# Performance work log

Hardware: AMD Instinct MI355X
Metric: run time of the kernel (lower is better)

Reference implementation:

```python
import jax, jax.numpy as jnp
import numpy as np

S, B, E = 2048, 8, 1024  # seq_len, batch, embed_dim
GAMMA = 0.5              # Kernel(gamma=0.5)


def setup_inputs() -> dict:
    key = jax.random.key(0)
    ks = jax.random.split(key, 4)
    # Weight scale 1/E keeps pairwise squared distances O(1) so the RBF
    # kernel weights are well-conditioned (exp doesn't underflow to all-zeros).
    w_scale = 1.0 / E
    inputs = jax.random.normal(ks[0], (S, B, E), dtype=jnp.float32)
    Wq = jax.random.normal(ks[1], (E, E), dtype=jnp.float32) * w_scale
    Wk = jax.random.normal(ks[2], (E, E), dtype=jnp.float32) * w_scale
    Wv = jax.random.normal(ks[3], (E, E), dtype=jnp.float32) * w_scale
    bq = jnp.zeros((E,), jnp.float32)
    bk = jnp.zeros((E,), jnp.float32)
    bv = jnp.zeros((E,), jnp.float32)
    return {"inputs": inputs, "Wq": Wq, "bq": bq, "Wk": Wk, "bk": bk,
            "Wv": Wv, "bv": bv}


def reference(inputs, Wq, bq, Wk, bk, Wv, bv):
    # QKV projections (nn.Linear: x @ W.T + b)
    q = inputs @ Wq.T + bq  # (S, B, E)
    k = inputs @ Wk.T + bk  # (S, B, E)
    v = inputs @ Wv.T + bv  # (S, B, E)

    # Pairwise RBF kernel sim[t, j, b] = exp(-gamma * ||q[t,b] - k[j,b]||^2)
    # (vectorized replacement of the original O(S^2) python double loop),
    # via ||q||^2 + ||k||^2 - 2 q.k expansion (GEMM-shaped contraction).
    q2 = jnp.sum(q * q, axis=-1)                 # (S, B)
    k2 = jnp.sum(k * k, axis=-1)                 # (S, B)
    qk = jnp.einsum('tbe,jbe->tjb', q, k)        # (S, S, B)
    d2 = q2[:, None, :] + k2[None, :, :] - 2.0 * qk
    d2 = jnp.maximum(d2, 0.0)

    # sim / sim.sum(dim=1) with sim = exp(-gamma*d2) is exactly
    # softmax(-gamma*d2) over axis 1 (the j axis) -- numerically stable form.
    sim = jax.nn.softmax(-GAMMA * d2, axis=1)    # (S, S, B): (t, j, b)

    # Aggregate values: out[t, b, e] = sum_j sim[t, j, b] * v[j, b, e]
    return jnp.einsum('tjb,jbe->tbe', sim, v)    # (S, B, E)
```

## Files before the change

kernel.cpp:

```cpp
#include <hip/hip_runtime.h>
#include <stdint.h>

#define S_LEN 2048
#define BATCH 8
#define EMB   1024
#define GAMMA 0.5f

typedef unsigned short ushort_t;
typedef __attribute__((ext_vector_type(8))) short  short8;
typedef __attribute__((ext_vector_type(8))) unsigned short ushort8;
typedef __attribute__((ext_vector_type(4))) float  floatx4;

__device__ __forceinline__ ushort_t f2bf(float f) {
  uint32_t x = __float_as_uint(f);
  x += 0x7fffu + ((x >> 16) & 1u);
  return (ushort_t)(x >> 16);
}

__device__ __forceinline__ void gl_lds16(const ushort_t* g, ushort_t* l) {
  __builtin_amdgcn_global_load_lds(
      (const __attribute__((address_space(1))) unsigned int*)g,
      (__attribute__((address_space(3))) unsigned int*)l, 16, 0, 0);
}


#define MFMA_16(AR, B0, B1, J0, J1)                                            \
  _Pragma("unroll")                                                            \
  for (int i = 0; i < 8; ++i) {                                                \
    acc[i][J0] = __builtin_amdgcn_mfma_f32_16x16x32_bf16(AR[i], B0, acc[i][J0], 0, 0, 0); \
    acc[i][J1] = __builtin_amdgcn_mfma_f32_16x16x32_bf16(AR[i], B1, acc[i][J1], 0, 0, 0); \
  }

#define PHASE_END()                                                            \
  asm volatile("s_waitcnt lgkmcnt(0)" ::: "memory");                           \
  __builtin_amdgcn_s_barrier();                                                \
  asm volatile("" ::: "memory");

__device__ __forceinline__ void gemm8_core(
    const ushort_t* __restrict__ A, const ushort_t* __restrict__ B,
    int lda, int ldb, int K, ushort_t* smem, floatx4 (&acc)[8][4])
{
  const int tid = threadIdx.x;
  const int wave = tid >> 6, lane = tid & 63;
  const int wm = wave >> 2, wn = wave & 3;
  const int lr = lane & 15, q = lane >> 4;
  const int NT = K >> 6;
  const int ra = wm * 128 + lr;
  const int rb = wn * 64 + lr;
  const int r4 = lane >> 2;
  const int slot = (lane & 3) ^ ((r4 >> 1) & 3);
  ushort_t* const lw = smem + wave * 1024;

  const int aOff = ra * 32 + (((q ^ (ra >> 1)) & 3) << 3);
  const int bOff = rb * 32 + (((q ^ (rb >> 1)) & 3) << 3);

  const ushort_t* pA0 = A + (size_t)(wave * 32 + r4) * lda + slot * 8;
  const ushort_t* pA1 = pA0 + (size_t)16 * lda;
  const ushort_t* pB0 = B + (size_t)(wave * 32 + r4) * ldb + slot * 8;
  const ushort_t* pB1 = pB0 + (size_t)16 * ldb;

  auto stA = [&](int regionOff, int koff) {
    gl_lds16(pA0 + koff, lw + regionOff);
    gl_lds16(pA1 + koff, lw + regionOff + 512);
  };
  auto stB = [&](int regionOff, int koff) {
    gl_lds16(pB0 + koff, lw + regionOff);
    gl_lds16(pB1 + koff, lw + regionOff + 512);
  };

  stA(0, 0);      stB(16384, 0);
  stA(8192, 32);  stB(24576, 32);
  stA(32768, 64); stB(49152, 64);
  stA(40960, 96);
  asm volatile("s_waitcnt vmcnt(6)" ::: "memory");
  __builtin_amdgcn_s_barrier();
  asm volatile("" ::: "memory");

  short8 ar[8], ar2[8], b0, b1, t0, t1, u0, u1;
  {
    const ushort_t* pa = smem + aOff;
    const ushort_t* pb = smem + 16384 + bOff;
#pragma unroll
    for (int i = 0; i < 8; ++i) ar[i] = *(const short8*)(pa + i * 512);
    b0 = *(const short8*)(pb);
    b1 = *(const short8*)(pb + 512);
  }

  for (int kt = 0; kt < NT; ++kt) {
    const int bo = (kt & 1) * 32768;
    const int bn = bo ^ 32768;
    const ushort_t* const curA0 = smem + bo + aOff;
    const ushort_t* const curA1 = smem + bo + 8192 + aOff;
    const ushort_t* const curB0 = smem + bo + 16384 + bOff;
    const ushort_t* const curB1 = smem + bo + 24576 + bOff;
    const ushort_t* const nxtA0 = smem + bn + aOff;
    const ushort_t* const nxtB0 = smem + bn + 16384 + bOff;
    const bool s1 = (kt + 1) < NT, s2 = (kt + 2) < NT;
    const int k1 = (kt + 1) << 6, k2 = (kt + 2) << 6;

    t0 = *(const short8*)(curB0 + 1024);
    t1 = *(const short8*)(curB0 + 1536);
#pragma unroll
    for (int i = 0; i < 4; ++i) ar2[i] = *(const short8*)(curA1 + i * 512);
    if (s1) stB(bn + 24576, k1 + 32);
    __builtin_amdgcn_s_setprio(1);
    MFMA_16(ar, b0, b1, 0, 1)
    __builtin_amdgcn_s_setprio(0);
    PHASE_END()

#pragma unroll
    for (int i = 4; i < 8; ++i) ar2[i] = *(const short8*)(curA1 + i * 512);
    u0 = *(const short8*)(curB1);
    u1 = *(const short8*)(curB1 + 512);
    if (s2) stA(bo, k2);
    __builtin_amdgcn_s_setprio(1);
    MFMA_16(ar, t0, t1, 2, 3)
    __builtin_amdgcn_s_setprio(0);
    PHASE_END()

    t0 = *(const short8*)(curB1 + 1024);
    t1 = *(const short8*)(curB1 + 1536);
    if (s2) stB(bo + 16384, k2);
    __builtin_amdgcn_s_setprio(1);
    MFMA_16(ar2, u0, u1, 0, 1)
    __builtin_amdgcn_s_setprio(0);
    if (s2)      { asm volatile("s_waitcnt vmcnt(4)" ::: "memory"); }
    else if (s1) { asm volatile("s_waitcnt vmcnt(0)" ::: "memory"); }
    PHASE_END()

    if (s1) {
#pragma unroll
      for (int i = 0; i < 8; ++i) ar[i] = *(const short8*)(nxtA0 + i * 512);
      b0 = *(const short8*)(nxtB0);
      b1 = *(const short8*)(nxtB0 + 512);
    }
    if (s2) stA(bo + 8192, k2 + 32);
    __builtin_amdgcn_s_setprio(1);
    MFMA_16(ar2, t0, t1, 2, 3)
    __builtin_amdgcn_s_setprio(0);
    PHASE_END()
  }
}

__global__ __launch_bounds__(256) void k_quant_x(const float* __restrict__ X,
                                                 ushort_t* __restrict__ Xb) {
  size_t i = ((size_t)blockIdx.x * 256 + threadIdx.x) * 4;
  float4 v = *(const float4*)(X + i);
  *(ushort4*)(Xb + i) = make_ushort4(f2bf(v.x), f2bf(v.y), f2bf(v.z), f2bf(v.w));
}

__global__ __launch_bounds__(256) void k_quant_w(
    const float* __restrict__ Wq, const float* __restrict__ Wk,
    const float* __restrict__ Wv, ushort_t* __restrict__ W) {
  size_t i = ((size_t)blockIdx.x * 256 + threadIdx.x) * 4;
  int row = (int)(i >> 10), col = (int)(i & 1023);
  int sel = row >> 10, sr = row & 1023;
  const float* src = sel == 0 ? Wq : (sel == 1 ? Wk : Wv);
  float4 v = *(const float4*)(src + (size_t)sr * 1024 + col);
  *(ushort4*)(W + i) = make_ushort4(f2bf(v.x), f2bf(v.y), f2bf(v.z), f2bf(v.w));
}

__global__ __launch_bounds__(256) void k_bias_zero(
    const float* __restrict__ bq, const float* __restrict__ bk,
    const float* __restrict__ bv, float* __restrict__ bias,
    float* __restrict__ q2, float* __restrict__ k2, float* __restrict__ rsum) {
  int i = blockIdx.x * 256 + threadIdx.x;
  if (i < 1024)       bias[i] = bq[i];
  else if (i < 2048)  bias[i] = bk[i - 1024];
  else if (i < 3072)  bias[i] = bv[i - 2048];
  if (i < BATCH * S_LEN) { q2[i] = 0.f; k2[i] = 0.f; rsum[i] = 0.f; }
}

__global__ __launch_bounds__(512, 2) void k_gemm_qkv(
    const ushort_t* __restrict__ Xb, const ushort_t* __restrict__ W,
    const float* __restrict__ bias,
    ushort_t* __restrict__ Q, ushort_t* __restrict__ Kp, ushort_t* __restrict__ V,
    float* __restrict__ q2, float* __restrict__ k2) {
  __shared__ __attribute__((aligned(16))) ushort_t smem[65536];
  const int lin = blockIdx.x + (blockIdx.y << 6);
  const int mt_i = (lin & 7) * 8 + ((lin >> 3) & 7);
  const int nt_i = lin >> 6;
  const int mt = mt_i * 256, nt = nt_i * 256;
  floatx4 acc[8][4];
  const floatx4 z = {0.f, 0.f, 0.f, 0.f};
#pragma unroll
  for (int i = 0; i < 8; ++i)
#pragma unroll
    for (int j = 0; j < 4; ++j) acc[i][j] = z;

  gemm8_core(Xb + (size_t)mt * EMB, W + (size_t)nt * EMB, EMB, EMB, EMB, smem, acc);

  const int lane = threadIdx.x & 63, wave = threadIdx.x >> 6;
  const int wm = wave >> 2, wn = wave & 3;
  const int lr = lane & 15, q = lane >> 4;
  const int which = nt >> 10;
  const int nc0 = nt & 1023;
  ushort_t* dst = which == 0 ? Q : (which == 1 ? Kp : V);
  float* sq = which == 0 ? q2 : k2;
  float bv4[4];
#pragma unroll
  for (int j = 0; j < 4; ++j) bv4[j] = bias[nt + wn * 64 + j * 16 + lr];

#pragma unroll
  for (int i = 0; i < 8; ++i) {
#pragma unroll
    for (int r = 0; r < 4; ++r) {
      const int g = mt + wm * 128 + i * 16 + q * 4 + r;
      const int t = g >> 3, b = g & 7;
      float ss = 0.f;
#pragma unroll
      for (int j = 0; j < 4; ++j) {
        const float val = acc[i][j][r] + bv4[j];
        dst[(size_t)(b * S_LEN + t) * EMB + nc0 + wn * 64 + j * 16 + lr] = f2bf(val);
        ss += val * val;
      }
      if (which < 2) {
        ss += __shfl_xor(ss, 1);
        ss += __shfl_xor(ss, 2);
        ss += __shfl_xor(ss, 4);
        ss += __shfl_xor(ss, 8);
        if (lr == 0) atomicAdd(&sq[b * S_LEN + t], ss);
      }
    }
  }
}

__global__ __launch_bounds__(256) void k_transpose(const ushort_t* __restrict__ V,
                                                   ushort_t* __restrict__ Vt) {
  __shared__ ushort_t tile[64][72];
  const int b = blockIdx.z, j0 = blockIdx.x * 64, e0 = blockIdx.y * 64;
  const ushort_t* src = V + ((size_t)b * S_LEN + j0) * EMB + e0;
  const int tid = threadIdx.x;
#pragma unroll
  for (int rep = 0; rep < 2; ++rep) {
    const int lin = rep * 256 + tid;
    const int j = lin >> 3, e8 = (lin & 7) * 8;
    *(uint4*)&tile[j][e8] = *(const uint4*)(src + (size_t)j * EMB + e8);
  }
  __syncthreads();
  ushort_t* dst = Vt + ((size_t)b * EMB + e0) * S_LEN + j0;
#pragma unroll
  for (int rep = 0; rep < 2; ++rep) {
    const int lin = rep * 256 + tid;
    const int e = lin >> 3, j8 = (lin & 7) * 8;
    ushort8 o;
#pragma unroll
    for (int m = 0; m < 8; ++m) o[m] = tile[j8 + m][e];
    *(ushort8*)(dst + (size_t)e * S_LEN + j8) = o;
  }
}

__global__ __launch_bounds__(512, 2) void k_logits(
    const ushort_t* __restrict__ Q, const ushort_t* __restrict__ Kp,
    const float* __restrict__ q2, const float* __restrict__ k2,
    ushort_t* __restrict__ P, float* __restrict__ rsum) {
  __shared__ __attribute__((aligned(16))) ushort_t smem[65536];
  const int lin = blockIdx.x + (blockIdx.y << 3) + (blockIdx.z << 6);
  const int b = lin & 7;
  const int seq = lin >> 3;
  const int mt = (seq & 7) * 256, nt = (seq >> 3) * 256;
  floatx4 acc[8][4];
  const floatx4 z = {0.f, 0.f, 0.f, 0.f};
#pragma unroll
  for (int i = 0; i < 8; ++i)
#pragma unroll
    for (int j = 0; j < 4; ++j) acc[i][j] = z;

  gemm8_core(Q + ((size_t)b * S_LEN + mt) * EMB,
             Kp + ((size_t)b * S_LEN + nt) * EMB, EMB, EMB, EMB, smem, acc);

  const int lane = threadIdx.x & 63, wave = threadIdx.x >> 6;
  const int wm = wave >> 2, wn = wave & 3;
  const int lr = lane & 15, q = lane >> 4;
  float k2v[4];
#pragma unroll
  for (int j = 0; j < 4; ++j) k2v[j] = k2[b * S_LEN + nt + wn * 64 + j * 16 + lr];

#pragma unroll
  for (int i = 0; i < 8; ++i) {
#pragma unroll
    for (int r = 0; r < 4; ++r) {
      const int t = mt + wm * 128 + i * 16 + q * 4 + r;
      const float q2v = q2[b * S_LEN + t];
      float ss = 0.f;
#pragma unroll
      for (int j = 0; j < 4; ++j) {
        float d2 = q2v + k2v[j] - 2.f * acc[i][j][r];
        d2 = fmaxf(d2, 0.f);
        const float p = __expf(-GAMMA * d2);
        P[((size_t)b * S_LEN + t) * S_LEN + nt + wn * 64 + j * 16 + lr] = f2bf(p);
        ss += p;
      }
      ss += __shfl_xor(ss, 1);
      ss += __shfl_xor(ss, 2);
      ss += __shfl_xor(ss, 4);
      ss += __shfl_xor(ss, 8);
      if (lr == 0) atomicAdd(&rsum[b * S_LEN + t], ss);
    }
  }
}

__global__ __launch_bounds__(512, 2) void k_out(
    const ushort_t* __restrict__ P, const ushort_t* __restrict__ Vt,
    const float* __restrict__ rsum, float* __restrict__ out) {
  __shared__ __attribute__((aligned(16))) ushort_t smem[65536];
  const int lin = blockIdx.x + (blockIdx.y << 3) + (blockIdx.z << 5);
  const int b = lin & 7;
  const int seq = lin >> 3;
  const int mt = (seq & 7) * 256, nt = (seq >> 3) * 256;
  floatx4 acc[8][4];
  const floatx4 z = {0.f, 0.f, 0.f, 0.f};
#pragma unroll
  for (int i = 0; i < 8; ++i)
#pragma unroll
    for (int j = 0; j < 4; ++j) acc[i][j] = z;

  gemm8_core(P + ((size_t)b * S_LEN + mt) * S_LEN,
             Vt + ((size_t)b * EMB + nt) * S_LEN, S_LEN, S_LEN, S_LEN, smem, acc);

  const int lane = threadIdx.x & 63, wave = threadIdx.x >> 6;
  const int wm = wave >> 2, wn = wave & 3;
  const int lr = lane & 15, q = lane >> 4;
#pragma unroll
  for (int i = 0; i < 8; ++i) {
#pragma unroll
    for (int r = 0; r < 4; ++r) {
      const int t = mt + wm * 128 + i * 16 + q * 4 + r;
      const float rinv = 1.f / rsum[b * S_LEN + t];
#pragma unroll
      for (int j = 0; j < 4; ++j) {
        const int e = nt + wn * 64 + j * 16 + lr;
        out[((size_t)t * BATCH + b) * EMB + e] = acc[i][j][r] * rinv;
      }
    }
  }
}

extern "C" void kernel_launch(void* const* d_in, const int* in_sizes, int n_in,
                              void* d_out, int out_size, void* d_ws, size_t ws_size,
                              hipStream_t stream) {
  (void)in_sizes; (void)n_in; (void)out_size; (void)ws_size;
  const float* X  = (const float*)d_in[0];
  const float* Wq = (const float*)d_in[1];
  const float* bq = (const float*)d_in[2];
  const float* Wk = (const float*)d_in[3];
  const float* bk = (const float*)d_in[4];
  const float* Wv = (const float*)d_in[5];
  const float* bv = (const float*)d_in[6];
  float* out = (float*)d_out;
  char* ws = (char*)d_ws;

  ushort_t* Q    = (ushort_t*)(ws + 0);
  ushort_t* Kp   = (ushort_t*)(ws + 33554432);
  ushort_t* V    = (ushort_t*)(ws + 67108864);
  ushort_t* Vt   = (ushort_t*)(ws + 100663296);
  ushort_t* P    = (ushort_t*)(ws + 134217728);
  ushort_t* Xb   = (ushort_t*)(ws + 134217728);
  ushort_t* Wqkv = (ushort_t*)(ws + 201326592);
  float*    bias = (float*)(ws + 207618048);
  float*    q2   = (float*)(ws + 207630336);
  float*    k2   = (float*)(ws + 207695872);
  float*    rsum = (float*)(ws + 207761408);

  k_quant_x <<<16384, 256, 0, stream>>>(X, Xb);
  k_quant_w <<<3072, 256, 0, stream>>>(Wq, Wk, Wv, Wqkv);
  k_bias_zero<<<64, 256, 0, stream>>>(bq, bk, bv, bias, q2, k2, rsum);
  k_gemm_qkv<<<dim3(64, 12), 512, 0, stream>>>(Xb, Wqkv, bias, Q, Kp, V, q2, k2);
  k_transpose<<<dim3(32, 16, 8), 256, 0, stream>>>(V, Vt);
  k_logits  <<<dim3(8, 8, 8), 512, 0, stream>>>(Q, Kp, q2, k2, P, rsum);
  k_out     <<<dim3(8, 4, 8), 512, 0, stream>>>(P, Vt, rsum, out);
}
```

Measured before the change: 399.8 us.

## Fuse V transpose into QKV GEMM epilogue and merge prep kernels

The three small preprocessing kernels (X quantize, W quantize, bias/zero init) are merged into one launch. The V projection tiles now go through a swizzled shared-memory transpose in the GEMM epilogue and are written straight to Vt. This removes the separate transpose kernel and the round trip through the intermediate V buffer. The cost is an extra __syncthreads and shared-memory traffic in the V-producing blocks, and the shared-memory layout reuses the GEMM buffer after the main loop.

```diff
diff --git a/kernel.cpp b/kernel.cpp
--- a/kernel.cpp
+++ b/kernel.cpp
@@ -89,7 +89,6 @@
   for (int kt = 0; kt < NT; ++kt) {
     const int bo = (kt & 1) * 32768;
     const int bn = bo ^ 32768;
-    const ushort_t* const curA0 = smem + bo + aOff;
     const ushort_t* const curA1 = smem + bo + 8192 + aOff;
     const ushort_t* const curB0 = smem + bo + 16384 + bOff;
     const ushort_t* const curB1 = smem + bo + 24576 + bOff;
@@ -142,39 +141,39 @@
   }
 }
 
-__global__ __launch_bounds__(256) void k_quant_x(const float* __restrict__ X,
-                                                 ushort_t* __restrict__ Xb) {
-  size_t i = ((size_t)blockIdx.x * 256 + threadIdx.x) * 4;
-  float4 v = *(const float4*)(X + i);
-  *(ushort4*)(Xb + i) = make_ushort4(f2bf(v.x), f2bf(v.y), f2bf(v.z), f2bf(v.w));
-}
-
-__global__ __launch_bounds__(256) void k_quant_w(
-    const float* __restrict__ Wq, const float* __restrict__ Wk,
-    const float* __restrict__ Wv, ushort_t* __restrict__ W) {
-  size_t i = ((size_t)blockIdx.x * 256 + threadIdx.x) * 4;
-  int row = (int)(i >> 10), col = (int)(i & 1023);
-  int sel = row >> 10, sr = row & 1023;
-  const float* src = sel == 0 ? Wq : (sel == 1 ? Wk : Wv);
-  float4 v = *(const float4*)(src + (size_t)sr * 1024 + col);
-  *(ushort4*)(W + i) = make_ushort4(f2bf(v.x), f2bf(v.y), f2bf(v.z), f2bf(v.w));
-}
-
-__global__ __launch_bounds__(256) void k_bias_zero(
+__global__ __launch_bounds__(256) void k_prep(
+    const float* __restrict__ X, const float* __restrict__ Wq,
+    const float* __restrict__ Wk, const float* __restrict__ Wv,
     const float* __restrict__ bq, const float* __restrict__ bk,
-    const float* __restrict__ bv, float* __restrict__ bias,
+    const float* __restrict__ bv,
+    ushort_t* __restrict__ Xb, ushort_t* __restrict__ W,
+    float* __restrict__ bias,
     float* __restrict__ q2, float* __restrict__ k2, float* __restrict__ rsum) {
-  int i = blockIdx.x * 256 + threadIdx.x;
-  if (i < 1024)       bias[i] = bq[i];
-  else if (i < 2048)  bias[i] = bk[i - 1024];
-  else if (i < 3072)  bias[i] = bv[i - 2048];
-  if (i < BATCH * S_LEN) { q2[i] = 0.f; k2[i] = 0.f; rsum[i] = 0.f; }
+  const int blk = blockIdx.x;
+  if (blk < 16384) {
+    size_t i = ((size_t)blk * 256 + threadIdx.x) * 4;
+    float4 v = *(const float4*)(X + i);
+    *(ushort4*)(Xb + i) = make_ushort4(f2bf(v.x), f2bf(v.y), f2bf(v.z), f2bf(v.w));
+  } else if (blk < 19456) {
+    size_t i = ((size_t)(blk - 16384) * 256 + threadIdx.x) * 4;
+    int row = (int)(i >> 10), col = (int)(i & 1023);
+    int sel = row >> 10, sr = row & 1023;
+    const float* src = sel == 0 ? Wq : (sel == 1 ? Wk : Wv);
+    float4 v = *(const float4*)(src + (size_t)sr * 1024 + col);
+    *(ushort4*)(W + i) = make_ushort4(f2bf(v.x), f2bf(v.y), f2bf(v.z), f2bf(v.w));
+  } else {
+    int i = (blk - 19456) * 256 + threadIdx.x;
+    if (i < 1024)       bias[i] = bq[i];
+    else if (i < 2048)  bias[i] = bk[i - 1024];
+    else if (i < 3072)  bias[i] = bv[i - 2048];
+    if (i < BATCH * S_LEN) { q2[i] = 0.f; k2[i] = 0.f; rsum[i] = 0.f; }
+  }
 }
 
 __global__ __launch_bounds__(512, 2) void k_gemm_qkv(
     const ushort_t* __restrict__ Xb, const ushort_t* __restrict__ W,
     const float* __restrict__ bias,
-    ushort_t* __restrict__ Q, ushort_t* __restrict__ Kp, ushort_t* __restrict__ V,
+    ushort_t* __restrict__ Q, ushort_t* __restrict__ Kp, ushort_t* __restrict__ Vt,
     float* __restrict__ q2, float* __restrict__ k2) {
   __shared__ __attribute__((aligned(16))) ushort_t smem[65536];
   const int lin = blockIdx.x + (blockIdx.y << 6);
@@ -190,31 +189,32 @@
 
   gemm8_core(Xb + (size_t)mt * EMB, W + (size_t)nt * EMB, EMB, EMB, EMB, smem, acc);
 
-  const int lane = threadIdx.x & 63, wave = threadIdx.x >> 6;
+  const int tid = threadIdx.x;
+  const int lane = tid & 63, wave = tid >> 6;
   const int wm = wave >> 2, wn = wave & 3;
   const int lr = lane & 15, q = lane >> 4;
   const int which = nt >> 10;
   const int nc0 = nt & 1023;
-  ushort_t* dst = which == 0 ? Q : (which == 1 ? Kp : V);
-  float* sq = which == 0 ? q2 : k2;
-  float bv4[4];
-#pragma unroll
-  for (int j = 0; j < 4; ++j) bv4[j] = bias[nt + wn * 64 + j * 16 + lr];
-
-#pragma unroll
-  for (int i = 0; i < 8; ++i) {
-#pragma unroll
-    for (int r = 0; r < 4; ++r) {
-      const int g = mt + wm * 128 + i * 16 + q * 4 + r;
-      const int t = g >> 3, b = g & 7;
-      float ss = 0.f;
-#pragma unroll
-      for (int j = 0; j < 4; ++j) {
-        const float val = acc[i][j][r] + bv4[j];
-        dst[(size_t)(b * S_LEN + t) * EMB + nc0 + wn * 64 + j * 16 + lr] = f2bf(val);
-        ss += val * val;
-      }
-      if (which < 2) {
+
+  if (which < 2) {
+    ushort_t* dst = which == 0 ? Q : Kp;
+    float* sq = which == 0 ? q2 : k2;
+    float bv4[4];
+#pragma unroll
+    for (int j = 0; j < 4; ++j) bv4[j] = bias[nt + wn * 64 + j * 16 + lr];
+#pragma unroll
+    for (int i = 0; i < 8; ++i) {
+#pragma unroll
+      for (int r = 0; r < 4; ++r) {
+        const int g = mt + wm * 128 + i * 16 + q * 4 + r;
+        const int t = g >> 3, b = g & 7;
+        float ss = 0.f;
+#pragma unroll
+        for (int j = 0; j < 4; ++j) {
+          const float val = acc[i][j][r] + bv4[j];
+          dst[(size_t)(b * S_LEN + t) * EMB + nc0 + wn * 64 + j * 16 + lr] = f2bf(val);
+          ss += val * val;
+        }
         ss += __shfl_xor(ss, 1);
         ss += __shfl_xor(ss, 2);
         ss += __shfl_xor(ss, 4);
@@ -222,31 +222,36 @@
         if (lr == 0) atomicAdd(&sq[b * S_LEN + t], ss);
       }
     }
-  }
-}
-
-__global__ __launch_bounds__(256) void k_transpose(const ushort_t* __restrict__ V,
-                                                   ushort_t* __restrict__ Vt) {
-  __shared__ ushort_t tile[64][72];
-  const int b = blockIdx.z, j0 = blockIdx.x * 64, e0 = blockIdx.y * 64;
-  const ushort_t* src = V + ((size_t)b * S_LEN + j0) * EMB + e0;
-  const int tid = threadIdx.x;
-#pragma unroll
-  for (int rep = 0; rep < 2; ++rep) {
-    const int lin = rep * 256 + tid;
-    const int j = lin >> 3, e8 = (lin & 7) * 8;
-    *(uint4*)&tile[j][e8] = *(const uint4*)(src + (size_t)j * EMB + e8);
-  }
-  __syncthreads();
-  ushort_t* dst = Vt + ((size_t)b * EMB + e0) * S_LEN + j0;
-#pragma unroll
-  for (int rep = 0; rep < 2; ++rep) {
-    const int lin = rep * 256 + tid;
-    const int e = lin >> 3, j8 = (lin & 7) * 8;
-    ushort8 o;
-#pragma unroll
-    for (int m = 0; m < 8; ++m) o[m] = tile[j8 + m][e];
-    *(ushort8*)(dst + (size_t)e * S_LEN + j8) = o;
+  } else {
+    float bv4[4];
+#pragma unroll
+    for (int j = 0; j < 4; ++j) bv4[j] = bias[nt + wn * 64 + j * 16 + lr];
+#pragma unroll
+    for (int i = 0; i < 8; ++i) {
+#pragma unroll
+      for (int r = 0; r < 4; ++r) {
+        const int l = wm * 128 + i * 16 + q * 4 + r;
+        const int tl = l >> 3, b = l & 7;
+#pragma unroll
+        for (int j = 0; j < 4; ++j) {
+          const int e = wn * 64 + j * 16 + lr;
+          smem[b * 8192 + e * 32 + (((tl >> 3) ^ (e & 3)) << 3) + (tl & 7)] =
+              f2bf(acc[i][j][r] + bv4[j]);
+        }
+      }
+    }
+    __syncthreads();
+    const int tb = mt >> 3;
+#pragma unroll
+    for (int rep = 0; rep < 16; ++rep) {
+      const int task = rep * 512 + tid;
+      const int quarter = task & 3;
+      const int pr = task >> 2;
+      const int e = pr & 255, b = pr >> 8;
+      const int chunk = quarter ^ (e & 3);
+      ushort8 vv = *(const ushort8*)(smem + b * 8192 + e * 32 + chunk * 8);
+      *(ushort8*)(Vt + ((size_t)b * EMB + nc0 + e) * S_LEN + tb + quarter * 8) = vv;
+    }
   }
 }
 
@@ -352,7 +357,6 @@
 
   ushort_t* Q    = (ushort_t*)(ws + 0);
   ushort_t* Kp   = (ushort_t*)(ws + 33554432);
-  ushort_t* V    = (ushort_t*)(ws + 67108864);
   ushort_t* Vt   = (ushort_t*)(ws + 100663296);
   ushort_t* P    = (ushort_t*)(ws + 134217728);
   ushort_t* Xb   = (ushort_t*)(ws + 134217728);
@@ -362,11 +366,9 @@
   float*    k2   = (float*)(ws + 207695872);
   float*    rsum = (float*)(ws + 207761408);
 
-  k_quant_x <<<16384, 256, 0, stream>>>(X, Xb);
-  k_quant_w <<<3072, 256, 0, stream>>>(Wq, Wk, Wv, Wqkv);
-  k_bias_zero<<<64, 256, 0, stream>>>(bq, bk, bv, bias, q2, k2, rsum);
-  k_gemm_qkv<<<dim3(64, 12), 512, 0, stream>>>(Xb, Wqkv, bias, Q, Kp, V, q2, k2);
-  k_transpose<<<dim3(32, 16, 8), 256, 0, stream>>>(V, Vt);
+  k_prep    <<<19520, 256, 0, stream>>>(X, Wq, Wk, Wv, bq, bk, bv,
+                                        Xb, Wqkv, bias, q2, k2, rsum);
+  k_gemm_qkv<<<dim3(64, 12), 512, 0, stream>>>(Xb, Wqkv, bias, Q, Kp, Vt, q2, k2);
   k_logits  <<<dim3(8, 8, 8), 512, 0, stream>>>(Q, Kp, q2, k2, P, rsum);
   k_out     <<<dim3(8, 4, 8), 512, 0, stream>>>(P, Vt, rsum, out);
 }
```

After: 377.6 us. -5.6%, faster.
